# Performance work log

Hardware: AMD Instinct MI355X
Metric: run time of the kernel (lower is better)

## Reference

```python
import jax, jax.numpy as jnp
import numpy as np

# Module config (matches init_kwargs)
SHAPE = (96, 128, 128)   # (D, H, W)
NUM_LAYERS = 2
K, S, P, DIL = 3, 2, 1, 1  # kernel, stride, padding, dilation (dilation=1)


def _sparse_maxpool(feat, mask):
    """One SparseMaxPool3d layer on a densified sparse tensor.

    feat: [B, D, H, W, C] float, inactive sites hold dtype-min
    mask: [B, D, H, W, 1] float 0/1 activity mask
    Max is taken only over ACTIVE input sites in each window (spconv semantics);
    an output site is active iff any input in its window is active.
    """
    neg = jnp.finfo(feat.dtype).min
    window = (1, K, K, K, 1)
    strides = (1, S, S, S, 1)
    pad = [(0, 0), (P, P), (P, P), (P, P), (0, 0)]
    masked = jnp.where(mask > 0, feat, neg)
    pooled = jax.lax.reduce_window(masked, neg, jax.lax.max, window, strides, pad)
    mask_out = jax.lax.reduce_window(mask, jnp.array(0, feat.dtype).item() * 0.0,
                                     jax.lax.max, window, strides, pad)
    return pooled, mask_out


def setup_inputs() -> dict:
    key = jax.random.key(0)
    k1, k2, k3, k4, k5 = jax.random.split(key, 5)
    N, C, B = 200000, 32, 2
    D, H, W = SHAPE
    features = jax.random.normal(k1, (N, C), dtype=jnp.float32)
    b = jax.random.randint(k2, (N,), 0, B)
    z = jax.random.randint(k3, (N,), 0, D)
    y = jax.random.randint(k4, (N,), 0, H)
    x = jax.random.randint(k5, (N,), 0, W)
    coors = jnp.stack([b, z, y, x], axis=1).astype(jnp.int32)
    return {"features": features, "coors": coors, "batch_size": B}


def reference(features, coors, batch_size):
    D, H, W = SHAPE
    C = features.shape[1]
    b, z, y, x = coors[:, 0], coors[:, 1], coors[:, 2], coors[:, 3]
    neg = jnp.finfo(features.dtype).min
    # Densify the sparse tensor (duplicate coords resolved by max, inactive = -inf)
    dense = jnp.full((batch_size, D, H, W, C), neg, features.dtype)
    dense = dense.at[b, z, y, x].max(features)
    mask = jnp.zeros((batch_size, D, H, W, 1), features.dtype).at[b, z, y, x].set(1.0)
    for _ in range(NUM_LAYERS):
        dense, mask = _sparse_maxpool(dense, mask)
    # Equivalent of SparseConvTensor.dense(): inactive output sites are 0
    return jnp.where(mask > 0, dense, jnp.zeros((), features.dtype))
```

## Files before the change

kernel.cpp:

```cpp
#include <hip/hip_runtime.h>
#include <cfloat>
#include <cstdint>

#define B_    2
#define OD    24
#define OH    32
#define OW    32
#define NC    32
#define NBINS (B_ * OD * OH * OW)
#define LINE  16
#define CAPR  15
#define OVF_CAP 100000
#define SCAN_T 1024
#define CHUNK  (NBINS / SCAN_T)

#define TZ 4
#define TY 4
#define TX 4
#define TCELLS (TZ*TY*TX)
#define NTZ (OD/TZ)
#define NTY (OH/TY)
#define NTX (OW/TX)
#define NTILES (B_*NTZ*NTY*NTX)
#define NBZ (TZ+1)
#define NBY (TY+1)
#define NBX (TX+1)
#define NB  (NBZ*NBY*NBX)
#define LIST_CAP 1792

__device__ __forceinline__ unsigned xform(float f) {
    unsigned u = __float_as_uint(f);
    return u ^ ((unsigned)((int)u >> 31) | 0x80000000u);
}
__device__ __forceinline__ float unxform(unsigned t) {
    return (t == 0u) ? 0.0f
           : __uint_as_float((t >> 31) ? (t ^ 0x80000000u) : ~t);
}


__global__ void k_zero(int* __restrict__ lines, int* __restrict__ ovf_n) {
    int i = blockIdx.x * blockDim.x + threadIdx.x;
    if (i < NBINS) lines[i * LINE] = 0;
    if (i == 0) *ovf_n = 0;
}

__global__ __launch_bounds__(256) void k_bin(const int* __restrict__ coors,
                                             int* __restrict__ lines,
                                             int* __restrict__ ovf_n,
                                             int2* __restrict__ ovf, int N) {
    int i = blockIdx.x * blockDim.x + threadIdx.x;
    if (i >= N) return;
    int4 cc = reinterpret_cast<const int4*>(coors)[i];
    int bin = (((cc.x * OD + (cc.y >> 2)) * OH + (cc.z >> 2)) * OW + (cc.w >> 2));
    int mask = 0xFF;
    if (!(cc.y & 3)) mask &= 0x55;
    if (!(cc.z & 3)) mask &= 0x33;
    if (!(cc.w & 3)) mask &= 0x0F;
    int rec = (i << 8) | mask;
    int pos = atomicAdd(&lines[bin * LINE], 1);
    if (pos < CAPR) {
        lines[bin * LINE + 1 + pos] = rec;
    } else {
        int o = atomicAdd(ovf_n, 1);
        if (o < OVF_CAP) ovf[o] = make_int2(bin, rec);
    }
}


__global__ __launch_bounds__(512) void k_tile(const float* __restrict__ feat,
                                              const int* __restrict__ lines,
                                              const int* __restrict__ ovf_n,
                                              const int2* __restrict__ ovf,
                                              float4* __restrict__ out4) {
    __shared__ unsigned sm_out[TCELLS * NC];
    __shared__ int2 list[LIST_CAP];
    __shared__ int sm_cursor;

    const int t   = blockIdx.x;
    const int tid = threadIdx.x;
    const int tx_ = t & (NTX - 1);
    const int ty_ = (t >> 3) & (NTY - 1);
    const int rest = t >> 6;
    const int b   = (rest >= NTZ) ? 1 : 0;
    const int tz_ = rest - b * NTZ;
    const int tz0 = tz_ * TZ, ty0 = ty_ * TY, tx0 = tx_ * TX;

    if (tid == 0) sm_cursor = 0;
    for (int v = tid; v < TCELLS * NC; v += 512) sm_out[v] = 0u;
    __syncthreads();

    if (tid < NB) {
        int rz  = tid / (NBY * NBX);
        int rem = tid - rz * (NBY * NBX);
        int ry  = rem / NBX;
        int rx  = rem - ry * NBX;
        int bz = tz0 - 1 + rz, by = ty0 - 1 + ry, bx = tx0 - 1 + rx;
        if ((bz | by | bx) >= 0) {
            int bin = ((b * OD + bz) * OH + by) * OW + bx;
            const int4* lp = (const int4*)(lines + bin * LINE);
            int4 q0 = lp[0], q1 = lp[1], q2 = lp[2], q3 = lp[3];
            int rbuf[16];
            *(int4*)&rbuf[0]  = q0; *(int4*)&rbuf[4]  = q1;
            *(int4*)&rbuf[8]  = q2; *(int4*)&rbuf[12] = q3;
            int cnt = rbuf[0]; if (cnt > CAPR) cnt = CAPR;
            int bi = rz - 1, bj = ry - 1, bl = rx - 1;
            int vm = 0xFF;
            if (bi < 0) vm &= 0xAA;  if (bi > TZ - 2) vm &= 0x55;
            if (bj < 0) vm &= 0xCC;  if (bj > TY - 2) vm &= 0x33;
            if (bl < 0) vm &= 0xF0;  if (bl > TX - 2) vm &= 0x0F;
            int cb = bi * (TY * TX) + bj * TX + bl;
            int nk = 0;
#pragma unroll
            for (int rs = 0; rs < CAPR; ++rs)
                if (rs < cnt && (rbuf[rs + 1] & vm & 0xFF)) ++nk;
            int pos = atomicAdd(&sm_cursor, nk);
#pragma unroll
            for (int rs = 0; rs < CAPR; ++rs) {
                if (rs < cnt) {
                    int rec = rbuf[rs + 1];
                    int fm = rec & vm & 0xFF;
                    if (fm) {
                        if (pos < LIST_CAP) {
                            list[pos] = make_int2((rec & ~0xFF) | fm, cb);
                        } else {
                            unsigned idx = ((unsigned)rec) >> 8;
                            for (int c2 = 0; c2 < NC; ++c2) {
                                unsigned tvv = xform(feat[idx * NC + c2]);
#pragma unroll
                                for (int k = 0; k < 8; ++k) {
                                    const int koff = ((k & 1) * (TY * TX)
                                        + ((k >> 1) & 1) * TX + ((k >> 2) & 1)) * NC;
                                    if ((fm >> k) & 1)
                                        atomicMax(&sm_out[(cb * NC) + koff + c2], tvv);
                                }
                            }
                        }
                        ++pos;
                    }
                }
            }
        }
    }

    int on = *ovf_n;
    if (on > 0 && tid == 0) {
        if (on > OVF_CAP) on = OVF_CAP;
        for (int e = 0; e < on; ++e) {
            int2 ov = ovf[e];
            int bx = ov.x & (OW - 1);
            int by = (ov.x >> 5) & (OH - 1);
            int rest2 = ov.x >> 10;
            int bb = (rest2 >= OD) ? 1 : 0;
            int bz = rest2 - bb * OD;
            if (bb != b) continue;
            int rz = bz - (tz0 - 1), ry = by - (ty0 - 1), rx = bx - (tx0 - 1);
            if (rz < 0 || rz >= NBZ || ry < 0 || ry >= NBY || rx < 0 || rx >= NBX) continue;
            int bi = rz - 1, bj = ry - 1, bl = rx - 1;
            int vm = 0xFF;
            if (bi < 0) vm &= 0xAA;  if (bi > TZ - 2) vm &= 0x55;
            if (bj < 0) vm &= 0xCC;  if (bj > TY - 2) vm &= 0x33;
            if (bl < 0) vm &= 0xF0;  if (bl > TX - 2) vm &= 0x0F;
            int fm = ov.y & vm & 0xFF;
            if (fm) {
                int pos = atomicAdd(&sm_cursor, 1);
                if (pos < LIST_CAP)
                    list[pos] = make_int2((ov.y & ~0xFF) | fm,
                                          bi * (TY * TX) + bj * TX + bl);
            }
        }
    }
    __syncthreads();
    int total = sm_cursor; if (total > LIST_CAP) total = LIST_CAP;

    const int s = tid >> 5;
    const int c = tid & 31;

    for (int j0 = s; j0 < total; j0 += 64) {
        int2 e0 = (j0      < total) ? list[j0]      : make_int2(0, 0);
        int2 e1 = (j0 + 16 < total) ? list[j0 + 16] : make_int2(0, 0);
        int2 e2 = (j0 + 32 < total) ? list[j0 + 32] : make_int2(0, 0);
        int2 e3 = (j0 + 48 < total) ? list[j0 + 48] : make_int2(0, 0);
        unsigned t0 = xform(feat[(((unsigned)e0.x) >> 8) * NC + c]);
        unsigned t1 = xform(feat[(((unsigned)e1.x) >> 8) * NC + c]);
        unsigned t2 = xform(feat[(((unsigned)e2.x) >> 8) * NC + c]);
        unsigned t3 = xform(feat[(((unsigned)e3.x) >> 8) * NC + c]);
#pragma unroll
        for (int k = 0; k < 8; ++k) {
            const int koff = ((k & 1) * (TY * TX) + ((k >> 1) & 1) * TX
                           + ((k >> 2) & 1)) * NC + c;
            if ((e0.x >> k) & 1) atomicMax(&sm_out[e0.y * NC + koff], t0);
            if ((e1.x >> k) & 1) atomicMax(&sm_out[e1.y * NC + koff], t1);
            if ((e2.x >> k) & 1) atomicMax(&sm_out[e2.y * NC + koff], t2);
            if ((e3.x >> k) & 1) atomicMax(&sm_out[e3.y * NC + koff], t3);
        }
    }
    __syncthreads();

    {
        const int cell = tid >> 3, quad = tid & 7;
        const int i = cell >> 4, jj = (cell >> 2) & 3, l = cell & 3;
        uint4 uv = *(const uint4*)&sm_out[cell * NC + quad * 4];
        float4 o;
        o.x = unxform(uv.x); o.y = unxform(uv.y);
        o.z = unxform(uv.z); o.w = unxform(uv.w);
        out4[(((size_t)(b * OD + tz0 + i) * OH + (ty0 + jj)) * OW
              + (tx0 + l)) * (NC / 4) + quad] = o;
    }
}


__global__ void k_hist(const int* __restrict__ coors, int* __restrict__ counts, int N) {
    int i = blockIdx.x * blockDim.x + threadIdx.x;
    if (i >= N) return;
    int4 cc = reinterpret_cast<const int4*>(coors)[i];
    int bin = (((cc.x * OD + (cc.y >> 2)) * OH + (cc.z >> 2)) * OW + (cc.w >> 2));
    atomicAdd(&counts[bin], 1);
}

__global__ void k_scan(const int* __restrict__ counts,
                       int2* __restrict__ binfo,
                       int* __restrict__ cursor) {
    __shared__ int lds[SCAN_T];
    int t = threadIdx.x;
    int base = t * CHUNK;
    int s = 0;
#pragma unroll
    for (int k = 0; k < CHUNK; ++k) s += counts[base + k];
    lds[t] = s;
    __syncthreads();
    for (int d = 1; d < SCAN_T; d <<= 1) {
        int v = (t >= d) ? lds[t - d] : 0;
        __syncthreads();
        lds[t] += v;
        __syncthreads();
    }
    int excl = (t == 0) ? 0 : lds[t - 1];
    for (int k = 0; k < CHUNK; ++k) {
        int i = base + k;
        int c = counts[i];
        binfo[i] = make_int2(excl, c);
        cursor[i] = excl;
        excl += c;
    }
}

__global__ void k_place(const int* __restrict__ coors, int* __restrict__ cursor,
                        int* __restrict__ records, int N) {
    int i = blockIdx.x * blockDim.x + threadIdx.x;
    if (i >= N) return;
    int4 cc = reinterpret_cast<const int4*>(coors)[i];
    int bin = (((cc.x * OD + (cc.y >> 2)) * OH + (cc.z >> 2)) * OW + (cc.w >> 2));
    int pos = atomicAdd(&cursor[bin], 1);
    records[pos] = (i << 6) | (cc.y & 3) | ((cc.z & 3) << 2) | ((cc.w & 3) << 4);
}

__global__ __launch_bounds__(256) void k_gather_fb(const float4* __restrict__ feat4,
                                                   const int2* __restrict__ binfo,
                                                   const int* __restrict__ records,
                                                   float4* __restrict__ out4, int N) {
    int tid  = blockIdx.x * blockDim.x + threadIdx.x;
    int wid  = tid >> 6;
    int lane = threadIdx.x & 63;
    int q    = lane >> 3;
    int cq   = lane & 7;

    int ox  = wid & (OW - 1);
    int oy  = (wid >> 5) & (OH - 1);
    int bzc = wid >> 10;
    int b   = (bzc >= OD) ? 1 : 0;
    int oz  = bzc - b * OD;

    int2 bi[8];
#pragma unroll
    for (int k = 0; k < 8; ++k) {
        const int lz = k & 1, ly = (k >> 1) & 1, lx = (k >> 2) & 1;
        int z2 = oz - lz, y2 = oy - ly, x2 = ox - lx;
        bool okbin = ((z2 | y2 | x2) >= 0);
        int bin = ((b * OD + z2) * OH + y2) * OW + x2;
        int2 v = binfo[okbin ? bin : 0];
        if (!okbin) { v.x = N; v.y = 0; }
        bi[k] = v;
    }

    int recs[8];
#pragma unroll
    for (int k = 0; k < 8; ++k) {
        int j = (q < bi[k].y) ? q : 0;
        recs[k] = records[bi[k].x + j];
    }

    float4 m = make_float4(-FLT_MAX, -FLT_MAX, -FLT_MAX, -FLT_MAX);
    int any = 0;
#pragma unroll
    for (int k = 0; k < 8; ++k) {
        int rec = recs[k];
        bool ok = (q < bi[k].y);
        if (k & 1) ok = ok && ((rec & 3)  != 0);
        if (k & 2) ok = ok && ((rec & 12) != 0);
        if (k & 4) ok = ok && ((rec & 48) != 0);
        if (ok) {
            float4 f = feat4[(rec >> 6) * (NC / 4) + cq];
            m.x = fmaxf(m.x, f.x); m.y = fmaxf(m.y, f.y);
            m.z = fmaxf(m.z, f.z); m.w = fmaxf(m.w, f.w);
            any = 1;
        }
    }

#pragma unroll
    for (int k = 0; k < 8; ++k) {
        for (int j0 = 8; j0 < bi[k].y; j0 += 8) {
            int j = j0 + q;
            bool ok = (j < bi[k].y);
            int rec = records[bi[k].x + (ok ? j : 0)];
            if (k & 1) ok = ok && ((rec & 3)  != 0);
            if (k & 2) ok = ok && ((rec & 12) != 0);
            if (k & 4) ok = ok && ((rec & 48) != 0);
            if (ok) {
                float4 f = feat4[(rec >> 6) * (NC / 4) + cq];
                m.x = fmaxf(m.x, f.x); m.y = fmaxf(m.y, f.y);
                m.z = fmaxf(m.z, f.z); m.w = fmaxf(m.w, f.w);
                any = 1;
            }
        }
    }

#pragma unroll
    for (int s = 8; s < 64; s <<= 1) {
        m.x = fmaxf(m.x, __shfl_xor(m.x, s, 64));
        m.y = fmaxf(m.y, __shfl_xor(m.y, s, 64));
        m.z = fmaxf(m.z, __shfl_xor(m.z, s, 64));
        m.w = fmaxf(m.w, __shfl_xor(m.w, s, 64));
    }
    bool active = (__ballot(any) != 0ULL);

    if (q == 0) {
        float4 z4 = make_float4(0.f, 0.f, 0.f, 0.f);
        out4[wid * (NC / 4) + cq] = active ? m : z4;
    }
}


extern "C" void kernel_launch(void* const* d_in, const int* in_sizes, int n_in,
                              void* d_out, int out_size, void* d_ws, size_t ws_size,
                              hipStream_t stream) {
    const float* feat  = (const float*)d_in[0];
    const int*   coors = (const int*)d_in[1];
    const int N = in_sizes[0] / NC;
    float* out = (float*)d_out;

    const size_t fast_ints = (size_t)NBINS * LINE + 8 + 2ull * OVF_CAP;
    if (ws_size >= fast_ints * sizeof(int)) {
        int*  lines = (int*)d_ws;
        int*  ovf_n = lines + NBINS * LINE;
        int2* ovf   = (int2*)(ovf_n + 8);

        k_zero<<<(NBINS + 255) / 256, 256, 0, stream>>>(lines, ovf_n);
        k_bin<<<(N + 255) / 256, 256, 0, stream>>>(coors, lines, ovf_n, ovf, N);
        k_tile<<<NTILES, 512, 0, stream>>>(feat, lines, ovf_n, (const int2*)ovf,
                                           (float4*)out);
    } else {
        int*  counts  = (int*)d_ws;
        int2* binfo   = (int2*)(counts + NBINS);
        int*  cursor  = (int*)(binfo + NBINS);
        int*  records = cursor + NBINS;

        hipMemsetAsync(counts, 0, NBINS * sizeof(int), stream);
        k_hist <<<(N + 255) / 256, 256, 0, stream>>>(coors, counts, N);
        k_scan <<<1, SCAN_T, 0, stream>>>(counts, binfo, cursor);
        k_place<<<(N + 255) / 256, 256, 0, stream>>>(coors, cursor, records, N);
        k_gather_fb<<<(NBINS * 64) / 256, 256, 0, stream>>>(
            (const float4*)feat, (const int2*)binfo, records, (float4*)out, N);
    }
}
```

Measured before the change: 43.51 us.

## Split bin counts from records, swizzle tile order, widen gather unroll

Bin counters move out of the 64-byte lines into their own compact array, cleared with hipMemsetAsync instead of a zero kernel, and records get a 16-slot stride. k_tile now uses two threads per neighbour bin, each taking alternating records, remaps block indices to interleave tiles across XCDs, and unrolls the feature gather to 8 list entries per iteration for more memory-level parallelism. The extra register pressure from the wider unroll and the separate counts load are the trade-offs.

```diff
diff --git a/kernel.cpp b/kernel.cpp
--- a/kernel.cpp
+++ b/kernel.cpp
@@ -8,8 +8,7 @@
 #define OW    32
 #define NC    32
 #define NBINS (B_ * OD * OH * OW)
-#define LINE  16
-#define CAPR  15
+#define RSTRIDE 16
 #define OVF_CAP 100000
 #define SCAN_T 1024
 #define CHUNK  (NBINS / SCAN_T)
@@ -38,14 +37,9 @@
 }
 
 
-__global__ void k_zero(int* __restrict__ lines, int* __restrict__ ovf_n) {
-    int i = blockIdx.x * blockDim.x + threadIdx.x;
-    if (i < NBINS) lines[i * LINE] = 0;
-    if (i == 0) *ovf_n = 0;
-}
-
 __global__ __launch_bounds__(256) void k_bin(const int* __restrict__ coors,
-                                             int* __restrict__ lines,
+                                             int* __restrict__ counts,
+                                             int* __restrict__ records,
                                              int* __restrict__ ovf_n,
                                              int2* __restrict__ ovf, int N) {
     int i = blockIdx.x * blockDim.x + threadIdx.x;
@@ -57,9 +51,9 @@
     if (!(cc.z & 3)) mask &= 0x33;
     if (!(cc.w & 3)) mask &= 0x0F;
     int rec = (i << 8) | mask;
-    int pos = atomicAdd(&lines[bin * LINE], 1);
-    if (pos < CAPR) {
-        lines[bin * LINE + 1 + pos] = rec;
+    int pos = atomicAdd(&counts[bin], 1);
+    if (pos < RSTRIDE) {
+        records[bin * RSTRIDE + pos] = rec;
     } else {
         int o = atomicAdd(ovf_n, 1);
         if (o < OVF_CAP) ovf[o] = make_int2(bin, rec);
@@ -68,7 +62,8 @@
 
 
 __global__ __launch_bounds__(512) void k_tile(const float* __restrict__ feat,
-                                              const int* __restrict__ lines,
+                                              const int* __restrict__ counts,
+                                              const int* __restrict__ records,
                                               const int* __restrict__ ovf_n,
                                               const int2* __restrict__ ovf,
                                               float4* __restrict__ out4) {
@@ -76,7 +71,7 @@
     __shared__ int2 list[LIST_CAP];
     __shared__ int sm_cursor;
 
-    const int t   = blockIdx.x;
+    const int t   = (blockIdx.x & 7) * (NTILES / 8) + (blockIdx.x >> 3);
     const int tid = threadIdx.x;
     const int tx_ = t & (NTX - 1);
     const int ty_ = (t >> 3) & (NTY - 1);
@@ -89,20 +84,21 @@
     for (int v = tid; v < TCELLS * NC; v += 512) sm_out[v] = 0u;
     __syncthreads();
 
-    if (tid < NB) {
-        int rz  = tid / (NBY * NBX);
-        int rem = tid - rz * (NBY * NBX);
+    if (tid < 2 * NB) {
+        int bn  = tid >> 1;
+        int par = tid & 1;
+        int rz  = bn / (NBY * NBX);
+        int rem = bn - rz * (NBY * NBX);
         int ry  = rem / NBX;
         int rx  = rem - ry * NBX;
         int bz = tz0 - 1 + rz, by = ty0 - 1 + ry, bx = tx0 - 1 + rx;
         if ((bz | by | bx) >= 0) {
             int bin = ((b * OD + bz) * OH + by) * OW + bx;
-            const int4* lp = (const int4*)(lines + bin * LINE);
-            int4 q0 = lp[0], q1 = lp[1], q2 = lp[2], q3 = lp[3];
+            int cnt = counts[bin]; if (cnt > RSTRIDE) cnt = RSTRIDE;
+            const int4* lp = (const int4*)(records + bin * RSTRIDE);
             int rbuf[16];
-            *(int4*)&rbuf[0]  = q0; *(int4*)&rbuf[4]  = q1;
-            *(int4*)&rbuf[8]  = q2; *(int4*)&rbuf[12] = q3;
-            int cnt = rbuf[0]; if (cnt > CAPR) cnt = CAPR;
+            *(int4*)&rbuf[0]  = lp[0]; *(int4*)&rbuf[4]  = lp[1];
+            *(int4*)&rbuf[8]  = lp[2]; *(int4*)&rbuf[12] = lp[3];
             int bi = rz - 1, bj = ry - 1, bl = rx - 1;
             int vm = 0xFF;
             if (bi < 0) vm &= 0xAA;  if (bi > TZ - 2) vm &= 0x55;
@@ -111,13 +107,13 @@
             int cb = bi * (TY * TX) + bj * TX + bl;
             int nk = 0;
 #pragma unroll
-            for (int rs = 0; rs < CAPR; ++rs)
-                if (rs < cnt && (rbuf[rs + 1] & vm & 0xFF)) ++nk;
+            for (int rs = 0; rs < RSTRIDE; ++rs)
+                if ((rs & 1) == par && rs < cnt && (rbuf[rs] & vm & 0xFF)) ++nk;
             int pos = atomicAdd(&sm_cursor, nk);
 #pragma unroll
-            for (int rs = 0; rs < CAPR; ++rs) {
-                if (rs < cnt) {
-                    int rec = rbuf[rs + 1];
+            for (int rs = 0; rs < RSTRIDE; ++rs) {
+                if ((rs & 1) == par && rs < cnt) {
+                    int rec = rbuf[rs];
                     int fm = rec & vm & 0xFF;
                     if (fm) {
                         if (pos < LIST_CAP) {
@@ -175,23 +171,25 @@
     const int s = tid >> 5;
     const int c = tid & 31;
 
-    for (int j0 = s; j0 < total; j0 += 64) {
-        int2 e0 = (j0      < total) ? list[j0]      : make_int2(0, 0);
-        int2 e1 = (j0 + 16 < total) ? list[j0 + 16] : make_int2(0, 0);
-        int2 e2 = (j0 + 32 < total) ? list[j0 + 32] : make_int2(0, 0);
-        int2 e3 = (j0 + 48 < total) ? list[j0 + 48] : make_int2(0, 0);
-        unsigned t0 = xform(feat[(((unsigned)e0.x) >> 8) * NC + c]);
-        unsigned t1 = xform(feat[(((unsigned)e1.x) >> 8) * NC + c]);
-        unsigned t2 = xform(feat[(((unsigned)e2.x) >> 8) * NC + c]);
-        unsigned t3 = xform(feat[(((unsigned)e3.x) >> 8) * NC + c]);
-#pragma unroll
-        for (int k = 0; k < 8; ++k) {
-            const int koff = ((k & 1) * (TY * TX) + ((k >> 1) & 1) * TX
-                           + ((k >> 2) & 1)) * NC + c;
-            if ((e0.x >> k) & 1) atomicMax(&sm_out[e0.y * NC + koff], t0);
-            if ((e1.x >> k) & 1) atomicMax(&sm_out[e1.y * NC + koff], t1);
-            if ((e2.x >> k) & 1) atomicMax(&sm_out[e2.y * NC + koff], t2);
-            if ((e3.x >> k) & 1) atomicMax(&sm_out[e3.y * NC + koff], t3);
+    for (int j0 = s; j0 < total; j0 += 128) {
+        int2 e[8];
+        unsigned tv[8];
+#pragma unroll
+        for (int u = 0; u < 8; ++u) {
+            int j = j0 + 16 * u;
+            e[u] = (j < total) ? list[j] : make_int2(0, 0);
+        }
+#pragma unroll
+        for (int u = 0; u < 8; ++u)
+            tv[u] = xform(feat[(((unsigned)e[u].x) >> 8) * NC + c]);
+#pragma unroll
+        for (int u = 0; u < 8; ++u) {
+#pragma unroll
+            for (int k = 0; k < 8; ++k) {
+                const int koff = ((k & 1) * (TY * TX) + ((k >> 1) & 1) * TX
+                               + ((k >> 2) & 1)) * NC + c;
+                if ((e[u].x >> k) & 1) atomicMax(&sm_out[e[u].y * NC + koff], tv[u]);
+            }
         }
     }
     __syncthreads();
@@ -348,16 +346,19 @@
     const int N = in_sizes[0] / NC;
     float* out = (float*)d_out;
 
-    const size_t fast_ints = (size_t)NBINS * LINE + 8 + 2ull * OVF_CAP;
+    const size_t fast_ints = (size_t)NBINS + 8 + (size_t)NBINS * RSTRIDE
+                           + 2ull * OVF_CAP;
     if (ws_size >= fast_ints * sizeof(int)) {
-        int*  lines = (int*)d_ws;
-        int*  ovf_n = lines + NBINS * LINE;
-        int2* ovf   = (int2*)(ovf_n + 8);
-
-        k_zero<<<(NBINS + 255) / 256, 256, 0, stream>>>(lines, ovf_n);
-        k_bin<<<(N + 255) / 256, 256, 0, stream>>>(coors, lines, ovf_n, ovf, N);
-        k_tile<<<NTILES, 512, 0, stream>>>(feat, lines, ovf_n, (const int2*)ovf,
-                                           (float4*)out);
+        int*  counts  = (int*)d_ws;
+        int*  ovf_n   = counts + NBINS;
+        int*  records = counts + NBINS + 8;
+        int2* ovf     = (int2*)(records + (size_t)NBINS * RSTRIDE);
+
+        hipMemsetAsync(counts, 0, (NBINS + 8) * sizeof(int), stream);
+        k_bin<<<(N + 255) / 256, 256, 0, stream>>>(coors, counts, records,
+                                                   ovf_n, ovf, N);
+        k_tile<<<NTILES, 512, 0, stream>>>(feat, counts, records,
+                                           ovf_n, (const int2*)ovf, (float4*)out);
     } else {
         int*  counts  = (int*)d_ws;
         int2* binfo   = (int2*)(counts + NBINS);
```

After: 43.24 us. About the same (-0.6%).
